# Kernel optimization log

Hardware: AMD Instinct MI355X
Metric: run time of the kernel (lower is better)

The kernel has to match this reference:

```python
import jax, jax.numpy as jnp
import numpy as np

B = 256        # graphs per batch (python loop in original, vectorized here)
N = 512        # nodes per graph
DEG = 16       # avg degree
E_PER = N * DEG
T = 64         # num_node_types
D = 128        # gnn_hidden_dim


def setup_inputs() -> dict:
    key = jax.random.key(0)
    ks = jax.random.split(key, 8)
    node_feat = jax.random.randint(ks[0], (B * N,), 0, T)
    offs = (jnp.arange(B) * N)[:, None]
    src = (jax.random.randint(ks[1], (B, E_PER), 0, N) + offs).reshape(-1)
    dst = (jax.random.randint(ks[2], (B, E_PER), 0, N) + offs).reshape(-1)
    emb_table = jax.random.normal(ks[3], (T, D), dtype=jnp.float32) * 0.02
    W1 = jax.random.normal(ks[4], (D, D), dtype=jnp.float32) * (1.0 / np.sqrt(D))
    b1 = jnp.zeros((D,), dtype=jnp.float32)
    W2 = jax.random.normal(ks[5], (D, D), dtype=jnp.float32) * (1.0 / np.sqrt(D))
    b2 = jnp.zeros((D,), dtype=jnp.float32)
    return {"node_feat": node_feat, "src": src, "dst": dst,
            "emb_table": emb_table, "W1": W1, "b1": b1, "W2": W2, "b2": b2}


def _gcn_layer(h, src, dst, out_isqrt, in_isqrt, W, b, n):
    # DGL GraphConv, norm='both': D_in^{-1/2} A D_out^{-1/2} h W + b
    m = (h * out_isqrt[:, None])[src]                      # [E, D] gather
    agg = jax.ops.segment_sum(m, dst, num_segments=n)      # [Ntot, D] scatter
    return (agg * in_isqrt[:, None]) @ W + b


def reference(node_feat, src, dst, emb_table, W1, b1, W2, b2):
    n = node_feat.shape[0]
    ones = jnp.ones(src.shape[0], dtype=emb_table.dtype)
    deg_out = jnp.clip(jax.ops.segment_sum(ones, src, num_segments=n), 1.0)
    deg_in = jnp.clip(jax.ops.segment_sum(ones, dst, num_segments=n), 1.0)
    out_isqrt = jax.lax.rsqrt(deg_out)
    in_isqrt = jax.lax.rsqrt(deg_in)

    h = emb_table[node_feat]                                # [Ntot, D]
    # layer 1 (dropout is eval-mode identity) + relu, layer 2 + relu
    h = jax.nn.relu(_gcn_layer(h, src, dst, out_isqrt, in_isqrt, W1, b1, n))
    h = jax.nn.relu(_gcn_layer(h, src, dst, out_isqrt, in_isqrt, W2, b2, n))

    # dgl.mean_nodes per graph, then mean_gnn_embeddings + stack -> [B, D]
    gid = jnp.arange(n) // N
    hg = jax.ops.segment_sum(h, gid, num_segments=B) / float(N)
    return hg
```

## Files before the change

kernel.cpp:

```cpp
#include <hip/hip_runtime.h>
#include <stdint.h>

#define GRAPHS 256
#define NPG    512
#define EPG    8192
#define NTOT   (GRAPHS*NPG)

typedef __attribute__((ext_vector_type(8))) short s16x8;
typedef __attribute__((ext_vector_type(4))) float f32x4;

__device__ __forceinline__ float bf2f(unsigned short u){
  union { unsigned int i; float f; } c; c.i = ((unsigned int)u)<<16; return c.f;
}
__device__ __forceinline__ unsigned short f2bf(float f){
  union { float f; unsigned int i; } c; c.f = f;
  unsigned int r = c.i + 0x7fffu + ((c.i>>16)&1u);
  return (unsigned short)(r>>16);
}

__global__ __launch_bounds__(512) void k_csr(const int* __restrict__ src,
      const int* __restrict__ dst, const int* __restrict__ ntype,
      const float* __restrict__ emb, const float* __restrict__ W1,
      unsigned short* __restrict__ sorted_g, int* __restrict__ start_g,
      float* __restrict__ out_isqrt, unsigned short* __restrict__ EW1T){
  __shared__ int hist[NPG], cursor[NPG], co[NPG], cs[NPG+1];
  __shared__ unsigned short ntype_sh[NPG];
  __shared__ unsigned short sorted[EPG];
  const int tid=threadIdx.x;
  if (blockIdx.x >= GRAPHS){
    const int gid = (blockIdx.x-GRAPHS)*512 + tid;
    const int t = gid>>7, c = gid&127;
    float acc=0.f;
    #pragma unroll 4
    for (int k=0;k<128;k++) acc += emb[t*128+k]*W1[k*128+c];
    EW1T[c*64+t]=f2bf(acc);
    return;
  }
  const int b=blockIdx.x, eb=b*EPG, nb=b*NPG;
  for (int v=tid; v<NPG; v+=512){
    hist[v]=0; co[v]=0; ntype_sh[v]=(unsigned short)ntype[nb+v];
  }
  __syncthreads();
  for (int i=tid;i<EPG;i+=512){
    atomicAdd(&hist[dst[eb+i]&(NPG-1)],1);
    atomicAdd(&co[src[eb+i]&(NPG-1)],1);
  }
  __syncthreads();
  if (tid<64){
    int carry=0;
    #pragma unroll
    for (int c=0;c<8;c++){
      int sc=hist[64*c+tid];
      #pragma unroll
      for (int off=1;off<64;off<<=1){ int y=__shfl_up(sc,off); if (tid>=off) sc+=y; }
      cs[64*c+tid+1]=carry+sc;
      carry+=__shfl(sc,63);
    }
    if (tid==0) cs[0]=0;
  }
  __syncthreads();
  for (int v=tid;v<NPG;v+=512) cursor[v]=cs[v];
  __syncthreads();
  for (int i=tid;i<EPG;i+=512){
    const int s=src[eb+i]&(NPG-1), d=dst[eb+i]&(NPG-1);
    const int pos=atomicAdd(&cursor[d],1);
    sorted[pos]=(unsigned short)((ntype_sh[s]<<9)|s);
  }
  __syncthreads();
  for (int i=tid;i<EPG/2;i+=512)
    ((unsigned int*)(sorted_g+(size_t)eb))[i] = ((const unsigned int*)sorted)[i];
  for (int v=tid;v<=NPG;v+=512) start_g[b*(NPG+1)+v]=cs[v];
  for (int v=tid;v<NPG;v+=512){
    int a=co[v]; if(a<1)a=1;
    out_isqrt[nb+v]=rsqrtf((float)a);
  }
}

#define A1_LDS 73232
__global__ __launch_bounds__(512) void k_agg1(
      const unsigned short* __restrict__ sorted_g, const int* __restrict__ start_g,
      const unsigned short* __restrict__ EW1T, const float* __restrict__ out_isqrt,
      const float* __restrict__ b1, unsigned short* __restrict__ h1F){
  extern __shared__ char smem[];
  float* S      = (float*)(smem);
  float* wsc    = (float*)(smem + 69632);
  int*   sstart = (int*)  (smem + 71680);
  float* bsh    = (float*)(smem + 72720);
  const int bid=blockIdx.x, b=bid>>1, half=bid&1;
  const int v0=half*256, nb=b*NPG, tid=threadIdx.x;
  for (int i=tid; i<(256*68)/4; i+=512) ((f32x4*)S)[i]=(f32x4){0.f,0.f,0.f,0.f};
  for (int i=tid; i<NPG; i+=512) wsc[i]=out_isqrt[nb+i];
  for (int i=tid; i<257; i+=512) sstart[i]=start_g[b*(NPG+1)+v0+i];
  if (tid<128) bsh[tid]=b1[tid];
  __syncthreads();
  if (tid<256){
    const int beg=sstart[tid], end=sstart[tid+1];
    float* Sd = S + tid*68;
    const unsigned short* sg = sorted_g + (size_t)b*EPG;
    for (int i=beg;i<end;++i){
      const int ent = sg[i];
      Sd[ent>>9] += wsc[ent&511];
    }
  }
  __syncthreads();
  const int wave=tid>>6, lane=tid&63, l16=lane&15, quad=lane>>4;
  f32x4 acc[2][8];
  #pragma unroll
  for (int rt=0;rt<2;rt++)
    #pragma unroll
    for (int nt=0;nt<8;nt++) acc[rt][nt]=(f32x4){0.f,0.f,0.f,0.f};
  #pragma unroll
  for (int ks=0; ks<4; ++ks){
    const int kc = (ks&1)*32 + quad*8;
    s16x8 a[2];
    #pragma unroll
    for (int rt=0;rt<2;rt++){
      const int m = (wave*2+rt)*16 + l16;
      const float* sp = &S[m*68 + kc];
      f32x4 va = *(const f32x4*)sp;
      f32x4 vb = *(const f32x4*)(sp+4);
      union { s16x8 v; unsigned short u[8]; } pk;
      #pragma unroll
      for (int j=0;j<8;j++){
        const float f = (j<4)? va[j] : vb[j-4];
        const unsigned short hi = f2bf(f);
        pk.u[j] = (ks<2) ? hi : f2bf(f - bf2f(hi));
      }
      a[rt]=pk.v;
    }
    #pragma unroll
    for (int nt=0;nt<8;nt++){
      s16x8 bfr=__builtin_bit_cast(s16x8,
          *(const uint4*)(EW1T + (size_t)(nt*16+l16)*64 + kc));
      #pragma unroll
      for (int rt=0;rt<2;rt++)
        acc[rt][nt]=__builtin_amdgcn_mfma_f32_16x16x32_bf16(a[rt],bfr,acc[rt][nt],0,0,0);
    }
  }
  #pragma unroll
  for (int rt=0;rt<2;rt++){
    const int W = wave*2+rt;
    const int mloc = W*16 + quad*4;
    float isq[4], os[4];
    #pragma unroll
    for (int r=0;r<4;r++){
      int d = sstart[mloc+r+1]-sstart[mloc+r]; if (d<1) d=1;
      isq[r]=rsqrtf((float)d);
      os[r]=wsc[v0+mloc+r];
    }
    const int ks2 = half*8 + (W>>1);
    const int q2  = ((W&1)<<1) | (quad>>1);
    const int j0  = (quad&1)*4;
    #pragma unroll
    for (int nt=0;nt<8;nt++){
      const int col = nt*16+l16;
      const float bb = bsh[col];
      ushort4 st;
      float v;
      v = fmaxf(acc[rt][nt][0]*isq[0]+bb,0.f)*os[0]; st.x=f2bf(v);
      v = fmaxf(acc[rt][nt][1]*isq[1]+bb,0.f)*os[1]; st.y=f2bf(v);
      v = fmaxf(acc[rt][nt][2]*isq[2]+bb,0.f)*os[2]; st.z=f2bf(v);
      v = fmaxf(acc[rt][nt][3]*isq[3]+bb,0.f)*os[3]; st.w=f2bf(v);
      const size_t off = ((((size_t)b*16 + ks2)*8 + nt)*64 + q2*16 + l16)*8 + j0;
      *(ushort4*)(h1F + off) = st;
    }
  }
}

#define A2_LDS 67080
__global__ __launch_bounds__(512) void k_agg2(
      const unsigned short* __restrict__ sorted_g, const int* __restrict__ start_g,
      const unsigned short* __restrict__ h1F, unsigned short* __restrict__ M1){
  extern __shared__ char smem[];
  unsigned char* A = (unsigned char*)smem;
  unsigned int* A32 = (unsigned int*)smem;
  int* sstart = (int*)(smem + 66560);
  const int bid=blockIdx.x;
  const int b  = ((bid>>5)<<3) | (bid&7);
  const int dt = (bid>>3)&3;
  const int v0=dt*128, nb=b*NPG, tid=threadIdx.x;
  for (int i=tid; i<66560/16; i+=512) ((uint4*)smem)[i]=(uint4){0u,0u,0u,0u};
  for (int i=tid; i<129; i+=512) sstart[i]=start_g[b*(NPG+1)+v0+i];
  __syncthreads();
  {
    const int d = tid>>2, q = tid&3;
    const int beg=sstart[d], end=sstart[d+1], len=end-beg;
    const int qb = beg + ((len*q)>>2), qe = beg + ((len*(q+1))>>2);
    const unsigned short* sg = sorted_g + (size_t)b*EPG;
    const int rowbase = d*130;
    for (int i=qb;i<qe;++i){
      const int s = sg[i]&511;
      atomicAdd(&A32[rowbase + (s>>2)], 1u<<((s&3)*8));
    }
  }
  __syncthreads();
  const int wave=tid>>6, lane=tid&63, l16=lane&15, quad=lane>>4;
  const int mg=wave>>1, ng=wave&1;
  f32x4 acc[2][4];
  #pragma unroll
  for (int rt=0;rt<2;rt++)
    #pragma unroll
    for (int ct=0;ct<4;ct++) acc[rt][ct]=(f32x4){0.f,0.f,0.f,0.f};

  const uint4* bp[4];
  #pragma unroll
  for (int ct=0;ct<4;ct++)
    bp[ct] = (const uint4*)h1F + (((size_t)b*16)*8 + (ng*4+ct))*64 + lane;
  const unsigned char* Ab[2];
  #pragma unroll
  for (int rt=0;rt<2;rt++)
    Ab[rt] = A + ((mg*2+rt)*16 + l16)*520 + quad*8;

  #pragma unroll 2
  for (int ks=0; ks<16; ++ks){
    uint4 bq[4];
    #pragma unroll
    for (int ct=0;ct<4;ct++) bq[ct] = bp[ct][(size_t)ks*512];
    s16x8 afr[2];
    #pragma unroll
    for (int rt=0;rt<2;rt++){
      const uint2 aw = *(const uint2*)(Ab[rt] + ks*32);
      union { s16x8 v; unsigned short u[8]; } pk;
      #pragma unroll
      for (int j=0;j<4;j++){
        const float f0 = (float)((aw.x>>(8*j))&0xffu);
        const float f1 = (float)((aw.y>>(8*j))&0xffu);
        pk.u[j]   = (unsigned short)(__builtin_bit_cast(unsigned int, f0)>>16);
        pk.u[j+4] = (unsigned short)(__builtin_bit_cast(unsigned int, f1)>>16);
      }
      afr[rt]=pk.v;
    }
    #pragma unroll
    for (int rt=0;rt<2;rt++)
      #pragma unroll
      for (int ct=0;ct<4;ct++)
        acc[rt][ct]=__builtin_amdgcn_mfma_f32_16x16x32_bf16(afr[rt],
            __builtin_bit_cast(s16x8, bq[ct]), acc[rt][ct],0,0,0);
  }
  #pragma unroll
  for (int rt=0;rt<2;rt++){
    const int mloc=(mg*2+rt)*16 + quad*4;
    float isq[4];
    #pragma unroll
    for (int r=0;r<4;r++){
      int d=sstart[mloc+r+1]-sstart[mloc+r]; if (d<1) d=1;
      isq[r]=rsqrtf((float)d);
    }
    #pragma unroll
    for (int ct=0;ct<4;ct++){
      const int col=ng*64 + ct*16 + l16;
      #pragma unroll
      for (int r=0;r<4;r++)
        M1[(size_t)(nb+v0+mloc+r)*128 + col] = f2bf(acc[rt][ct][r]*isq[r]);
    }
  }
}

__global__ __launch_bounds__(512) void k_gemm2(const unsigned short* __restrict__ M1,
      const float* __restrict__ W2, const float* __restrict__ b2,
      float* __restrict__ out){
  __shared__ __align__(16) unsigned short WT[128][136];
  __shared__ float bsh[128];
  __shared__ float colpart[8][128];
  const int b=blockIdx.x, tid=threadIdx.x;
  for (int idx=tid; idx<128*128; idx+=512){
    const int k=idx>>7, n=idx&127;
    WT[n][k]=f2bf(W2[idx]);
  }
  if (tid<128) bsh[tid]=b2[tid];
  __syncthreads();
  const int wave=tid>>6, lane=tid&63, l16=lane&15, quad=lane>>4;
  float p[8];
  #pragma unroll
  for (int i=0;i<8;i++) p[i]=0.f;
  for (int chunk=0; chunk<2; ++chunk){
    const int rowbase = b*NPG + wave*64 + chunk*32;
    f32x4 acc[2][8];
    #pragma unroll
    for (int rt=0;rt<2;rt++)
      #pragma unroll
      for (int ct=0;ct<8;ct++) acc[rt][ct]=(f32x4){0.f,0.f,0.f,0.f};
    #pragma unroll
    for (int ks=0;ks<4;ks++){
      s16x8 a[2], bf[8];
      #pragma unroll
      for (int rt=0;rt<2;rt++){
        const unsigned short* ap = M1 + (size_t)(rowbase+rt*16+l16)*128 + ks*32 + quad*8;
        a[rt]=__builtin_bit_cast(s16x8, *(const uint4*)ap);
      }
      #pragma unroll
      for (int ct=0;ct<8;ct++)
        bf[ct]=__builtin_bit_cast(s16x8, *(const uint4*)&WT[ct*16+l16][ks*32+quad*8]);
      #pragma unroll
      for (int rt=0;rt<2;rt++)
        #pragma unroll
        for (int ct=0;ct<8;ct++)
          acc[rt][ct]=__builtin_amdgcn_mfma_f32_16x16x32_bf16(a[rt],bf[ct],acc[rt][ct],0,0,0);
    }
    #pragma unroll
    for (int rt=0;rt<2;rt++)
      #pragma unroll
      for (int ct=0;ct<8;ct++)
        #pragma unroll
        for (int r=0;r<4;r++){
          const int col=ct*16+l16;
          p[ct] += fmaxf(acc[rt][ct][r]+bsh[col],0.f);
        }
  }
  #pragma unroll
  for (int ct=0;ct<8;ct++){
    p[ct] += __shfl_xor(p[ct],16);
    p[ct] += __shfl_xor(p[ct],32);
  }
  if (quad==0){
    #pragma unroll
    for (int ct=0;ct<8;ct++) colpart[wave][ct*16+l16]=p[ct];
  }
  __syncthreads();
  if (tid<128){
    float s=0.f;
    #pragma unroll
    for (int w=0;w<8;w++) s+=colpart[w][tid];
    out[b*128+tid]=s*(1.f/512.f);
  }
}

extern "C" void kernel_launch(void* const* d_in, const int* in_sizes, int n_in,
                              void* d_out, int out_size, void* d_ws, size_t ws_size,
                              hipStream_t stream){
  const int* node_feat = (const int*)d_in[0];
  const int* src = (const int*)d_in[1];
  const int* dst = (const int*)d_in[2];
  const float* emb = (const float*)d_in[3];
  const float* W1  = (const float*)d_in[4];
  const float* b1  = (const float*)d_in[5];
  const float* W2  = (const float*)d_in[6];
  const float* b2  = (const float*)d_in[7];

  char* ws = (char*)d_ws;
  float* out_isqrt        = (float*)(ws);
  int* start_g            = (int*)(ws + 524288);
  unsigned short* sorted_g= (unsigned short*)(ws + 1049600);
  unsigned short* EW1T    = (unsigned short*)(ws + 5243904);
  unsigned short* h1F     = (unsigned short*)(ws + 5260288);
  unsigned short* M1      = (unsigned short*)(ws + 38814720);

  (void)hipFuncSetAttribute(reinterpret_cast<const void*>(&k_agg1),
        hipFuncAttributeMaxDynamicSharedMemorySize, A1_LDS);
  (void)hipFuncSetAttribute(reinterpret_cast<const void*>(&k_agg2),
        hipFuncAttributeMaxDynamicSharedMemorySize, A2_LDS);

  k_csr<<<GRAPHS+16,512,0,stream>>>(src,dst,node_feat,emb,W1,
        sorted_g,start_g,out_isqrt,EW1T);
  k_agg1<<<GRAPHS*2,512,A1_LDS,stream>>>(sorted_g,start_g,EW1T,out_isqrt,b1,h1F);
  k_agg2<<<GRAPHS*4,512,A2_LDS,stream>>>(sorted_g,start_g,h1F,M1);
  k_gemm2<<<GRAPHS,512,0,stream>>>(M1,W2,b2,(float*)d_out);
}
```

Before: 151.8 us.

## Store M1 in MFMA fragment layout and vectorize edge loads in CSR build

The intermediate M1 matrix is now written by the second aggregation kernel directly in the per-lane MFMA A-fragment order, so the final GEMM reads each fragment as one contiguous 16-byte load per lane instead of strided row reads. The CSR build kernel also loads src/dst as int4 once into registers and reuses them for both the histogram and the scatter pass, avoiding a second global read of the edge lists. The writes in agg2 become scattered 2-byte stores at a different stride, which may cost some store efficiency.

```diff
diff --git a/kernel.cpp b/kernel.cpp
--- a/kernel.cpp
+++ b/kernel.cpp
@@ -37,13 +37,21 @@
     return;
   }
   const int b=blockIdx.x, eb=b*EPG, nb=b*NPG;
-  for (int v=tid; v<NPG; v+=512){
-    hist[v]=0; co[v]=0; ntype_sh[v]=(unsigned short)ntype[nb+v];
-  }
-  __syncthreads();
-  for (int i=tid;i<EPG;i+=512){
-    atomicAdd(&hist[dst[eb+i]&(NPG-1)],1);
-    atomicAdd(&co[src[eb+i]&(NPG-1)],1);
+  hist[tid]=0; co[tid]=0; ntype_sh[tid]=(unsigned short)ntype[nb+tid];
+  __syncthreads();
+  int4 d4[4], s4[4];
+  {
+    const int4* dv = (const int4*)(dst+eb);
+    const int4* sv = (const int4*)(src+eb);
+    #pragma unroll
+    for (int j=0;j<4;j++){
+      d4[j]=dv[tid + j*512];
+      s4[j]=sv[tid + j*512];
+      atomicAdd(&hist[d4[j].x&(NPG-1)],1); atomicAdd(&hist[d4[j].y&(NPG-1)],1);
+      atomicAdd(&hist[d4[j].z&(NPG-1)],1); atomicAdd(&hist[d4[j].w&(NPG-1)],1);
+      atomicAdd(&co[s4[j].x&(NPG-1)],1);   atomicAdd(&co[s4[j].y&(NPG-1)],1);
+      atomicAdd(&co[s4[j].z&(NPG-1)],1);   atomicAdd(&co[s4[j].w&(NPG-1)],1);
+    }
   }
   __syncthreads();
   if (tid<64){
@@ -59,20 +67,28 @@
     if (tid==0) cs[0]=0;
   }
   __syncthreads();
-  for (int v=tid;v<NPG;v+=512) cursor[v]=cs[v];
-  __syncthreads();
-  for (int i=tid;i<EPG;i+=512){
-    const int s=src[eb+i]&(NPG-1), d=dst[eb+i]&(NPG-1);
-    const int pos=atomicAdd(&cursor[d],1);
-    sorted[pos]=(unsigned short)((ntype_sh[s]<<9)|s);
+  cursor[tid]=cs[tid];
+  __syncthreads();
+  #pragma unroll
+  for (int j=0;j<4;j++){
+    int dl, s, pos;
+    dl=d4[j].x&(NPG-1); s=s4[j].x&(NPG-1);
+    pos=atomicAdd(&cursor[dl],1); sorted[pos]=(unsigned short)((ntype_sh[s]<<9)|s);
+    dl=d4[j].y&(NPG-1); s=s4[j].y&(NPG-1);
+    pos=atomicAdd(&cursor[dl],1); sorted[pos]=(unsigned short)((ntype_sh[s]<<9)|s);
+    dl=d4[j].z&(NPG-1); s=s4[j].z&(NPG-1);
+    pos=atomicAdd(&cursor[dl],1); sorted[pos]=(unsigned short)((ntype_sh[s]<<9)|s);
+    dl=d4[j].w&(NPG-1); s=s4[j].w&(NPG-1);
+    pos=atomicAdd(&cursor[dl],1); sorted[pos]=(unsigned short)((ntype_sh[s]<<9)|s);
   }
   __syncthreads();
   for (int i=tid;i<EPG/2;i+=512)
     ((unsigned int*)(sorted_g+(size_t)eb))[i] = ((const unsigned int*)sorted)[i];
-  for (int v=tid;v<=NPG;v+=512) start_g[b*(NPG+1)+v]=cs[v];
-  for (int v=tid;v<NPG;v+=512){
-    int a=co[v]; if(a<1)a=1;
-    out_isqrt[nb+v]=rsqrtf((float)a);
+  if (tid==0) start_g[b*(NPG+1)+NPG]=cs[NPG];
+  start_g[b*(NPG+1)+tid]=cs[tid];
+  {
+    int a=co[tid]; if(a<1)a=1;
+    out_isqrt[nb+tid]=rsqrtf((float)a);
   }
 }
 
@@ -170,7 +186,7 @@
 #define A2_LDS 67080
 __global__ __launch_bounds__(512) void k_agg2(
       const unsigned short* __restrict__ sorted_g, const int* __restrict__ start_g,
-      const unsigned short* __restrict__ h1F, unsigned short* __restrict__ M1){
+      const unsigned short* __restrict__ h1F, unsigned short* __restrict__ M1F){
   extern __shared__ char smem[];
   unsigned char* A = (unsigned char*)smem;
   unsigned int* A32 = (unsigned int*)smem;
@@ -178,7 +194,7 @@
   const int bid=blockIdx.x;
   const int b  = ((bid>>5)<<3) | (bid&7);
   const int dt = (bid>>3)&3;
-  const int v0=dt*128, nb=b*NPG, tid=threadIdx.x;
+  const int v0=dt*128, tid=threadIdx.x;
   for (int i=tid; i<66560/16; i+=512) ((uint4*)smem)[i]=(uint4){0u,0u,0u,0u};
   for (int i=tid; i<129; i+=512) sstart[i]=start_g[b*(NPG+1)+v0+i];
   __syncthreads();
@@ -240,6 +256,7 @@
   #pragma unroll
   for (int rt=0;rt<2;rt++){
     const int mloc=(mg*2+rt)*16 + quad*4;
+    const int M = dt*8 + mg*2 + rt;
     float isq[4];
     #pragma unroll
     for (int r=0;r<4;r++){
@@ -248,15 +265,19 @@
     }
     #pragma unroll
     for (int ct=0;ct<4;ct++){
-      const int col=ng*64 + ct*16 + l16;
+      const int ks2   = ng*2 + (ct>>1);
+      const int quad2 = ((ct&1)<<1) | (l16>>3);
+      const int j     = l16&7;
+      unsigned short* base = M1F
+          + ((((size_t)b*32+M)*4+ks2)*64 + quad2*16)*8 + j;
       #pragma unroll
       for (int r=0;r<4;r++)
-        M1[(size_t)(nb+v0+mloc+r)*128 + col] = f2bf(acc[rt][ct][r]*isq[r]);
-    }
-  }
-}
-
-__global__ __launch_bounds__(512) void k_gemm2(const unsigned short* __restrict__ M1,
+        base[(size_t)(quad*4+r)*8] = f2bf(acc[rt][ct][r]*isq[r]);
+    }
+  }
+}
+
+__global__ __launch_bounds__(512) void k_gemm2(const unsigned short* __restrict__ M1F,
       const float* __restrict__ W2, const float* __restrict__ b2,
       float* __restrict__ out){
   __shared__ __align__(16) unsigned short WT[128][136];
@@ -274,7 +295,6 @@
   #pragma unroll
   for (int i=0;i<8;i++) p[i]=0.f;
   for (int chunk=0; chunk<2; ++chunk){
-    const int rowbase = b*NPG + wave*64 + chunk*32;
     f32x4 acc[2][8];
     #pragma unroll
     for (int rt=0;rt<2;rt++)
@@ -285,8 +305,9 @@
       s16x8 a[2], bf[8];
       #pragma unroll
       for (int rt=0;rt<2;rt++){
-        const unsigned short* ap = M1 + (size_t)(rowbase+rt*16+l16)*128 + ks*32 + quad*8;
-        a[rt]=__builtin_bit_cast(s16x8, *(const uint4*)ap);
+        const int M = wave*4 + chunk*2 + rt;
+        a[rt]=__builtin_bit_cast(s16x8, *(const uint4*)(M1F
+            + ((((size_t)b*32+M)*4+ks)*64 + lane)*8));
       }
       #pragma unroll
       for (int ct=0;ct<8;ct++)
@@ -343,7 +364,7 @@
   unsigned short* sorted_g= (unsigned short*)(ws + 1049600);
   unsigned short* EW1T    = (unsigned short*)(ws + 5243904);
   unsigned short* h1F     = (unsigned short*)(ws + 5260288);
-  unsigned short* M1      = (unsigned short*)(ws + 38814720);
+  unsigned short* M1F     = (unsigned short*)(ws + 38814720);
 
   (void)hipFuncSetAttribute(reinterpret_cast<const void*>(&k_agg1),
         hipFuncAttributeMaxDynamicSharedMemorySize, A1_LDS);
@@ -353,6 +374,6 @@
   k_csr<<<GRAPHS+16,512,0,stream>>>(src,dst,node_feat,emb,W1,
         sorted_g,start_g,out_isqrt,EW1T);
   k_agg1<<<GRAPHS*2,512,A1_LDS,stream>>>(sorted_g,start_g,EW1T,out_isqrt,b1,h1F);
-  k_agg2<<<GRAPHS*4,512,A2_LDS,stream>>>(sorted_g,start_g,h1F,M1);
-  k_gemm2<<<GRAPHS,512,0,stream>>>(M1,W2,b2,(float*)d_out);
-}
+  k_agg2<<<GRAPHS*4,512,A2_LDS,stream>>>(sorted_g,start_g,h1F,M1F);
+  k_gemm2<<<GRAPHS,512,0,stream>>>(M1F,W2,b2,(float*)d_out);
+}
```

After: 150.0 us. Within noise of the previous version (-1.2%).
